# Kernel optimization log

Measured on AMD Instinct MI355X. Metric: run time of the kernel, lower is better.

## Reference

```python
import jax, jax.numpy as jnp
import numpy as np

B, C, H, W = 1, 256, 64, 64
K_DIM, V_DIM, HEADS = 64, 64, 8


def setup_inputs() -> dict:
    key = jax.random.key(0)
    ks = jax.random.split(key, 13)
    s = lambda i, shape: jax.random.normal(ks[i], shape, dtype=jnp.float32) * 0.05
    return {
        "x": s(0, (B, C, H, W)),
        # low-rank bottleneck projections (bias=False), torch Linear weight is [out,in]
        "wq1": s(1, (K_DIM // 2, C)),
        "wk1": s(2, (K_DIM // 2, C)),
        "wv1": s(3, (V_DIM // 2, C)),
        # expansion to per-head dims (bias=False)
        "wq2": s(4, (K_DIM * HEADS, K_DIM // 2)),
        "wk2": s(5, (K_DIM * HEADS, K_DIM // 2)),
        "wv2": s(6, (V_DIM * HEADS, V_DIM // 2)),
        # output projection (with bias)
        "wo": s(7, (C, V_DIM * HEADS)),
        "bo": s(8, (C,)),
        # depthwise 3x3 conv (groups=C): [C,1,3,3]
        "w_dw": s(9, (C, 1, 3, 3)),
        "b_dw": s(10, (C,)),
        # 1x1 gate conv
        "w_gate": s(11, (C, C, 1, 1)),
        "b_gate": s(12, (C,)),
    }


def reference(x, wq1, wk1, wv1, wq2, wk2, wv2, wo, bo, w_dw, b_dw, w_gate, b_gate):
    B_, C_, H_, W_ = x.shape
    N = H_ * W_
    t = x.transpose(0, 2, 3, 1).reshape(B_, N, C_)  # [B, N, C]
    # low-rank then expansion: Linear(x) = x @ W.T
    q = (t @ wq1.T) @ wq2.T  # [B, N, HEADS*K_DIM]
    k = (t @ wk1.T) @ wk2.T
    v = (t @ wv1.T) @ wv2.T
    q = q.reshape(B_, N, HEADS, K_DIM).transpose(0, 2, 1, 3)  # [B,h,N,dk]
    k = k.reshape(B_, N, HEADS, K_DIM).transpose(0, 2, 1, 3)
    v = v.reshape(B_, N, HEADS, V_DIM).transpose(0, 2, 1, 3)
    attn = jnp.einsum('bhnd,bhmd->bhnm', q, k) / jnp.sqrt(jnp.float32(K_DIM))
    attn = jax.nn.softmax(attn, axis=-1)
    out = jnp.einsum('bhnm,bhmd->bhnd', attn, v)  # [B,h,N,dv]
    out = out.transpose(0, 2, 1, 3).reshape(B_, N, HEADS * V_DIM)
    out = out @ wo.T + bo  # [B, N, C]
    out = out.reshape(B_, H_, W_, C_).transpose(0, 3, 1, 2)  # NCHW
    dn = ('NCHW', 'OIHW', 'NCHW')
    out = jax.lax.conv_general_dilated(out, w_dw, (1, 1), 'SAME', dimension_numbers=dn,
                                       feature_group_count=C_) + b_dw[None, :, None, None]
    gate = jax.nn.sigmoid(
        jax.lax.conv_general_dilated(out, w_gate, (1, 1), 'SAME', dimension_numbers=dn)
        + b_gate[None, :, None, None])
    return out * gate
```

## Files before the change

kernel.cpp:

```cpp
#include <hip/hip_runtime.h>

typedef __bf16 bf16;
typedef __bf16 bf16x4 __attribute__((ext_vector_type(4)));
typedef __bf16 bf16x8 __attribute__((ext_vector_type(8)));
typedef float f32x4 __attribute__((ext_vector_type(4)));

#define MFMA16(a, b, c) __builtin_amdgcn_mfma_f32_16x16x32_bf16((a), (b), (c), 0, 0, 0)

__device__ inline float fexp2(float x) {
    float r;
    asm("v_exp_f32 %0, %1" : "=v"(r) : "v"(x));
    return r;
}

__global__ void k_transpose_x(const float* __restrict__ x, bf16* __restrict__ xt) {
    __shared__ float tile[64][68];
    const int t = threadIdx.x;
    const int c0 = (blockIdx.x & 3) * 64;
    const int n0 = (blockIdx.x >> 2) * 64;
    {
        const int cr = t >> 4, nc = (t & 15) * 4;
#pragma unroll
        for (int i = 0; i < 4; ++i) {
            const float4 v = *(const float4*)(x + (size_t)(c0 + cr + i * 16) * 4096 + n0 + nc);
            tile[cr + i * 16][nc + 0] = v.x;
            tile[cr + i * 16][nc + 1] = v.y;
            tile[cr + i * 16][nc + 2] = v.z;
            tile[cr + i * 16][nc + 3] = v.w;
        }
    }
    __syncthreads();
    const int n = t >> 2, cc = (t & 3) * 16;
    bf16x8 o0, o1;
#pragma unroll
    for (int j = 0; j < 8; ++j) o0[j] = (bf16)tile[cc + j][n];
#pragma unroll
    for (int j = 0; j < 8; ++j) o1[j] = (bf16)tile[cc + 8 + j][n];
    bf16* dst = xt + (size_t)(n0 + n) * 256 + c0 + cc;
    *(bf16x8*)dst = o0;
    *(bf16x8*)(dst + 8) = o1;
}

__global__ void k_prep_w(const float* __restrict__ wq1, const float* __restrict__ wk1,
                         const float* __restrict__ wv1, const float* __restrict__ wq2,
                         const float* __restrict__ wk2, const float* __restrict__ wv2,
                         const float* __restrict__ wo, const float* __restrict__ wg,
                         bf16* __restrict__ Wq, bf16* __restrict__ Wk, bf16* __restrict__ Wv,
                         bf16* __restrict__ wo_bf, bf16* __restrict__ wg_bf) {
    int t = blockIdx.x * 256 + threadIdx.x;
    if (t < 393216) {
        int which = t >> 17;
        int rem = t & 131071;
        int o = rem >> 8, c = rem & 255;
        const float* w1 = which == 0 ? wq1 : which == 1 ? wk1 : wv1;
        const float* w2 = which == 0 ? wq2 : which == 1 ? wk2 : wv2;
        float acc = 0.f;
#pragma unroll
        for (int j = 0; j < 32; ++j) acc += w2[o * 32 + j] * w1[j * 256 + c];
        bf16* W = which == 0 ? Wq : which == 1 ? Wk : Wv;
        W[o * 256 + c] = (bf16)acc;
    } else if (t < 524288) {
        int idx = t - 393216;
        wo_bf[idx] = (bf16)wo[idx];
    } else if (t < 589824) {
        int idx = t - 524288;
        wg_bf[idx] = (bf16)wg[idx];
    }
}

template <int MODE>
__launch_bounds__(256)
__global__ void k_gemm_nt(const bf16* __restrict__ A, const bf16* __restrict__ B,
                          int K, float scale, void* __restrict__ outp,
                          const float* __restrict__ bias, const float* __restrict__ mul) {
    const int lane = threadIdx.x & 63;
    const int w = threadIdx.x >> 6;
    const int i0 = blockIdx.y * 128 + w * 32;
    const int j0 = blockIdx.x * 64;
    const int lrow = lane & 15;
    const int lk = (lane >> 4) * 8;

    f32x4 acc[2][4];
#pragma unroll
    for (int a = 0; a < 2; ++a)
#pragma unroll
        for (int b = 0; b < 4; ++b) acc[a][b] = (f32x4){0.f, 0.f, 0.f, 0.f};

    for (int k0 = 0; k0 < K; k0 += 32) {
        bf16x8 af[2], bfr[4];
#pragma unroll
        for (int qs = 0; qs < 2; ++qs)
            af[qs] = *(const bf16x8*)(A + (size_t)(i0 + qs * 16 + lrow) * K + k0 + lk);
#pragma unroll
        for (int js = 0; js < 4; ++js)
            bfr[js] = *(const bf16x8*)(B + (size_t)(j0 + js * 16 + lrow) * K + k0 + lk);
#pragma unroll
        for (int qs = 0; qs < 2; ++qs)
#pragma unroll
            for (int js = 0; js < 4; ++js)
                acc[qs][js] = MFMA16(af[qs], bfr[js], acc[qs][js]);
    }

    const int rbase = (lane >> 4) * 4;
#pragma unroll
    for (int qs = 0; qs < 2; ++qs)
#pragma unroll
        for (int js = 0; js < 4; ++js)
#pragma unroll
            for (int r = 0; r < 4; ++r) {
                int i = i0 + qs * 16 + rbase + r;
                int j = j0 + js * 16 + lrow;
                float v = acc[qs][js][r];
                if (MODE == 0) {
                    ((bf16*)outp)[(size_t)(j >> 6) * (4096 * 64) + (size_t)i * 64 + (j & 63)] =
                        (bf16)(v * scale);
                } else if (MODE == 1) {
                    ((bf16*)outp)[(size_t)i * 4096 + j] = (bf16)v;
                } else if (MODE == 2) {
                    ((float*)outp)[(size_t)i * 4096 + j] = v + bias[i];
                } else {
                    float g = v + bias[i];
                    float sg = 1.f / (1.f + __expf(-g));
                    ((float*)outp)[(size_t)i * 4096 + j] = mul[(size_t)i * 4096 + j] * sg;
                }
            }
}

__launch_bounds__(256)
__global__ void k_attn(const bf16* __restrict__ q, const bf16* __restrict__ k,
                       const bf16* __restrict__ vT, bf16* __restrict__ Opart,
                       float* __restrict__ lpart) {
    __shared__ char kvlds[16384];
    __shared__ char plds[4][4096];
    const int tid = threadIdx.x;
    const int lane = tid & 63;
    const int w = tid >> 6;
    const int split = blockIdx.x >> 8;
    const int h = (blockIdx.x >> 5) & 7;
    const int qt = blockIdx.x & 31;
    const int qbase = qt * 128 + w * 32;
    const int lrow = lane & 15;
    const int g = lane >> 4;
    const int swzr = (lrow & 7) << 4;

    const bf16* qh = q + (size_t)h * 4096 * 64;
    const bf16* kh = k + (size_t)h * 4096 * 64;
    const bf16* vh = vT + (size_t)h * 64 * 4096;
    char* myp = plds[w];
    const char* Kl = kvlds;
    const char* Vl = kvlds + 8192;

    const int isV = tid >> 7;
    const int srow = (tid & 127) >> 1;
    const int shalf = tid & 1;
    const int swzs = (srow & 7) << 4;
    char* ldst = kvlds + isV * 8192 + srow * 128;
    const bf16* sbase = isV ? (vh + (size_t)srow * 4096 + split * 1024 + shalf * 32)
                            : (kh + ((size_t)split * 1024 + srow) * 64 + shalf * 32);
    const size_t sstep = isV ? 64 : 64 * 64;

    bf16x8 bq[2][2];
#pragma unroll
    for (int qs = 0; qs < 2; ++qs)
#pragma unroll
        for (int ks = 0; ks < 2; ++ks)
            bq[qs][ks] = *(const bf16x8*)(qh + (size_t)(qbase + qs * 16 + lrow) * 64 +
                                          ks * 32 + g * 8);

    f32x4 accO[2][4];
    float lsum[2] = {0.f, 0.f};
#pragma unroll
    for (int qs = 0; qs < 2; ++qs)
#pragma unroll
        for (int ds = 0; ds < 4; ++ds) accO[qs][ds] = (f32x4){0.f, 0.f, 0.f, 0.f};

    uint4 r0, r1, r2, r3;
    {
        const bf16* p = sbase;
        r0 = *(const uint4*)(p);
        r1 = *(const uint4*)(p + 8);
        r2 = *(const uint4*)(p + 16);
        r3 = *(const uint4*)(p + 24);
    }

    for (int t = 0; t < 16; ++t) {
        *(uint4*)(ldst + ((shalf * 64 + 0) ^ swzs)) = r0;
        *(uint4*)(ldst + ((shalf * 64 + 16) ^ swzs)) = r1;
        *(uint4*)(ldst + ((shalf * 64 + 32) ^ swzs)) = r2;
        *(uint4*)(ldst + ((shalf * 64 + 48) ^ swzs)) = r3;
        if (t < 15) {
            const bf16* p = sbase + (size_t)(t + 1) * sstep;
            r0 = *(const uint4*)(p);
            r1 = *(const uint4*)(p + 8);
            r2 = *(const uint4*)(p + 16);
            r3 = *(const uint4*)(p + 24);
        }
        __syncthreads();

#pragma unroll
        for (int qs = 0; qs < 2; ++qs) {
            const int qrow = qs * 16 + lrow;
            f32x4 s[4];
#pragma unroll
            for (int js = 0; js < 4; ++js) s[js] = (f32x4){0.f, 0.f, 0.f, 0.f};
#pragma unroll
            for (int ks = 0; ks < 2; ++ks) {
                bf16x8 ak[4];
#pragma unroll
                for (int js = 0; js < 4; ++js)
                    ak[js] = *(const bf16x8*)(Kl + (js * 16 + lrow) * 128 +
                                              ((ks * 64 + g * 16) ^ swzr));
#pragma unroll
                for (int js = 0; js < 4; ++js)
                    s[js] = MFMA16(ak[js], bq[qs][ks], s[js]);
            }
#pragma unroll
            for (int js = 0; js < 4; ++js) {
                bf16x4 pk;
#pragma unroll
                for (int r = 0; r < 4; ++r) {
                    float e = fexp2(s[js][r]);
                    lsum[qs] += e;
                    pk[r] = (bf16)e;
                }
                *(bf16x4*)(myp + ((qrow * 128 + js * 32 + g * 8) ^ swzr)) = pk;
            }
#pragma unroll
            for (int ks2 = 0; ks2 < 2; ++ks2) {
                bf16x8 ap = *(const bf16x8*)(myp + ((qrow * 128 + ks2 * 64 + g * 16) ^ swzr));
                bf16x8 bv[4];
#pragma unroll
                for (int ds = 0; ds < 4; ++ds)
                    bv[ds] = *(const bf16x8*)(Vl + (ds * 16 + lrow) * 128 +
                                              ((ks2 * 64 + g * 16) ^ swzr));
#pragma unroll
                for (int ds = 0; ds < 4; ++ds)
                    accO[qs][ds] = MFMA16(ap, bv[ds], accO[qs][ds]);
            }
        }
        __syncthreads();
    }

#pragma unroll
    for (int qs = 0; qs < 2; ++qs)
#pragma unroll
        for (int ds = 0; ds < 4; ++ds)
#pragma unroll
            for (int r = 0; r < 4; ++r) {
                const int n = qbase + qs * 16 + 4 * g + r;
                Opart[((size_t)split * 4096 + n) * 512 + h * 64 + ds * 16 + lrow] =
                    (bf16)accO[qs][ds][r];
            }
#pragma unroll
    for (int qs = 0; qs < 2; ++qs) {
        float lv = lsum[qs];
        lv += __shfl_xor(lv, 16);
        lv += __shfl_xor(lv, 32);
        if (lane < 16)
            lpart[((size_t)split * 8 + h) * 4096 + qbase + qs * 16 + lane] = lv;
    }
}

__global__ void k_combine(const bf16* __restrict__ Opart, const float* __restrict__ lpart,
                          bf16* __restrict__ o) {
    const int tid = blockIdx.x * 256 + threadIdx.x;
    const int n = tid >> 6;
    const int c8 = (tid & 63) * 8;
    const int h = c8 >> 6;
    float acc[8] = {0, 0, 0, 0, 0, 0, 0, 0};
    float l = 0.f;
#pragma unroll
    for (int s = 0; s < 4; ++s) {
        const bf16x8 v = *(const bf16x8*)(Opart + ((size_t)s * 4096 + n) * 512 + c8);
#pragma unroll
        for (int j = 0; j < 8; ++j) acc[j] += (float)v[j];
        l += lpart[((size_t)s * 8 + h) * 4096 + n];
    }
    const float inv = 1.f / l;
    bf16x8 ov;
#pragma unroll
    for (int j = 0; j < 8; ++j) ov[j] = (bf16)(acc[j] * inv);
    *(bf16x8*)(o + (size_t)n * 512 + c8) = ov;
}

__global__ void k_dw(const float* __restrict__ y, const float* __restrict__ wdw,
                     const float* __restrict__ bdw, float* __restrict__ dwout,
                     bf16* __restrict__ dwt) {
    int t = blockIdx.x * 256 + threadIdx.x;
    int c = t >> 12, n = t & 4095, yy = n >> 6, xx = n & 63;
    float acc = bdw[c];
    const float* yc = y + (size_t)c * 4096;
#pragma unroll
    for (int ky = 0; ky < 3; ++ky) {
        int ry = yy + ky - 1;
        if ((unsigned)ry < 64u) {
#pragma unroll
            for (int kx = 0; kx < 3; ++kx) {
                int rx = xx + kx - 1;
                if ((unsigned)rx < 64u) acc += wdw[c * 9 + ky * 3 + kx] * yc[ry * 64 + rx];
            }
        }
    }
    dwout[t] = acc;
    dwt[n * 256 + c] = (bf16)acc;
}

extern "C" void kernel_launch(void* const* d_in, const int* in_sizes, int n_in,
                              void* d_out, int out_size, void* d_ws, size_t ws_size,
                              hipStream_t stream) {
    const float* x   = (const float*)d_in[0];
    const float* wq1 = (const float*)d_in[1];
    const float* wk1 = (const float*)d_in[2];
    const float* wv1 = (const float*)d_in[3];
    const float* wq2 = (const float*)d_in[4];
    const float* wk2 = (const float*)d_in[5];
    const float* wv2 = (const float*)d_in[6];
    const float* wo  = (const float*)d_in[7];
    const float* bo  = (const float*)d_in[8];
    const float* wdw = (const float*)d_in[9];
    const float* bdw = (const float*)d_in[10];
    const float* wg  = (const float*)d_in[11];
    const float* bg  = (const float*)d_in[12];

    char* ws = (char*)d_ws;
    size_t off = 0;
    auto alloc = [&](size_t bytes) {
        char* p = ws + off;
        off += (bytes + 255) & ~(size_t)255;
        return p;
    };
    bf16*  q_buf = (bf16*)alloc((size_t)8 * 4096 * 64 * 2);
    bf16*  k_buf = (bf16*)alloc((size_t)8 * 4096 * 64 * 2);
    bf16*  vT    = (bf16*)alloc((size_t)8 * 64 * 4096 * 2);
    bf16*  o_buf = (bf16*)alloc((size_t)4096 * 512 * 2);
    bf16*  wo_bf = (bf16*)alloc((size_t)256 * 512 * 2);
    bf16*  wg_bf = (bf16*)alloc((size_t)256 * 256 * 2);
    char* U = ws + off;
    bf16*  xbf = (bf16*)U;
    bf16*  Wq  = (bf16*)(U + (size_t)2 * 1024 * 1024);
    bf16*  Wk  = (bf16*)(U + (size_t)2 * 1024 * 1024 + 262144);
    bf16*  Wv  = (bf16*)(U + (size_t)2 * 1024 * 1024 + 524288);
    bf16*  Opart = (bf16*)U;
    float* lpart = (float*)(U + (size_t)16 * 1024 * 1024);
    float* ybuf  = (float*)U;
    float* dwout = (float*)(U + (size_t)4 * 1024 * 1024);
    bf16*  dwt   = (bf16*)(U + (size_t)8 * 1024 * 1024);
    (void)ws_size; (void)in_sizes; (void)n_in; (void)out_size;

    const float QSCALE = 0.125f * 1.4426950408889634f;

    k_transpose_x<<<256, 256, 0, stream>>>(x, xbf);
    k_prep_w<<<2304, 256, 0, stream>>>(wq1, wk1, wv1, wq2, wk2, wv2, wo, wg,
                                       Wq, Wk, Wv, wo_bf, wg_bf);
    k_gemm_nt<0><<<dim3(8, 32), 256, 0, stream>>>(xbf, Wq, 256, QSCALE, q_buf, nullptr, nullptr);
    k_gemm_nt<0><<<dim3(8, 32), 256, 0, stream>>>(xbf, Wk, 256, 1.0f, k_buf, nullptr, nullptr);
    k_gemm_nt<1><<<dim3(64, 4), 256, 0, stream>>>(Wv, xbf, 256, 1.0f, vT, nullptr, nullptr);
    k_attn<<<1024, 256, 0, stream>>>(q_buf, k_buf, vT, Opart, lpart);
    k_combine<<<1024, 256, 0, stream>>>(Opart, lpart, o_buf);
    k_gemm_nt<2><<<dim3(64, 2), 256, 0, stream>>>(wo_bf, o_buf, 512, 1.0f, ybuf, bo, nullptr);
    k_dw<<<4096, 256, 0, stream>>>(ybuf, wdw, bdw, dwout, dwt);
    k_gemm_nt<3><<<dim3(64, 2), 256, 0, stream>>>(wg_bf, dwt, 256, 1.0f, d_out, bg, dwout);
}
```

Baseline: 128.1 us.

## Double-buffer K/V tiles in attention, MFMA row sums, merge prep kernels

The attention kernel now double-buffers its K/V shared-memory tiles. The next tile is written into the alternate buffer while the current one is consumed, which removes one barrier per iteration. The per-row softmax denominator is now accumulated with an extra MFMA against a vector of ones instead of scalar adds in the exp loop. This takes VALU work off the loop but uses the bf16-rounded probabilities for the sum. The x-transpose and weight-prep kernels are merged into one launch to save a kernel launch. Shared memory grows by 16 KB per block, which may reduce occupancy.

Result: no change. 127.0 us (-0.9%).

```diff
diff --git a/kernel.cpp b/kernel.cpp
--- a/kernel.cpp
+++ b/kernel.cpp
@@ -13,58 +13,60 @@
     return r;
 }
 
-__global__ void k_transpose_x(const float* __restrict__ x, bf16* __restrict__ xt) {
+__global__ void k_pre(const float* __restrict__ x, bf16* __restrict__ xt,
+                      const float* __restrict__ wq1, const float* __restrict__ wk1,
+                      const float* __restrict__ wv1, const float* __restrict__ wq2,
+                      const float* __restrict__ wk2, const float* __restrict__ wv2,
+                      const float* __restrict__ wo, const float* __restrict__ wg,
+                      bf16* __restrict__ Wq, bf16* __restrict__ Wk, bf16* __restrict__ Wv,
+                      bf16* __restrict__ wo_bf, bf16* __restrict__ wg_bf) {
     __shared__ float tile[64][68];
-    const int t = threadIdx.x;
-    const int c0 = (blockIdx.x & 3) * 64;
-    const int n0 = (blockIdx.x >> 2) * 64;
-    {
-        const int cr = t >> 4, nc = (t & 15) * 4;
-#pragma unroll
-        for (int i = 0; i < 4; ++i) {
-            const float4 v = *(const float4*)(x + (size_t)(c0 + cr + i * 16) * 4096 + n0 + nc);
-            tile[cr + i * 16][nc + 0] = v.x;
-            tile[cr + i * 16][nc + 1] = v.y;
-            tile[cr + i * 16][nc + 2] = v.z;
-            tile[cr + i * 16][nc + 3] = v.w;
-        }
-    }
-    __syncthreads();
-    const int n = t >> 2, cc = (t & 3) * 16;
-    bf16x8 o0, o1;
-#pragma unroll
-    for (int j = 0; j < 8; ++j) o0[j] = (bf16)tile[cc + j][n];
-#pragma unroll
-    for (int j = 0; j < 8; ++j) o1[j] = (bf16)tile[cc + 8 + j][n];
-    bf16* dst = xt + (size_t)(n0 + n) * 256 + c0 + cc;
-    *(bf16x8*)dst = o0;
-    *(bf16x8*)(dst + 8) = o1;
-}
-
-__global__ void k_prep_w(const float* __restrict__ wq1, const float* __restrict__ wk1,
-                         const float* __restrict__ wv1, const float* __restrict__ wq2,
-                         const float* __restrict__ wk2, const float* __restrict__ wv2,
-                         const float* __restrict__ wo, const float* __restrict__ wg,
-                         bf16* __restrict__ Wq, bf16* __restrict__ Wk, bf16* __restrict__ Wv,
-                         bf16* __restrict__ wo_bf, bf16* __restrict__ wg_bf) {
-    int t = blockIdx.x * 256 + threadIdx.x;
-    if (t < 393216) {
-        int which = t >> 17;
-        int rem = t & 131071;
-        int o = rem >> 8, c = rem & 255;
-        const float* w1 = which == 0 ? wq1 : which == 1 ? wk1 : wv1;
-        const float* w2 = which == 0 ? wq2 : which == 1 ? wk2 : wv2;
-        float acc = 0.f;
-#pragma unroll
-        for (int j = 0; j < 32; ++j) acc += w2[o * 32 + j] * w1[j * 256 + c];
-        bf16* W = which == 0 ? Wq : which == 1 ? Wk : Wv;
-        W[o * 256 + c] = (bf16)acc;
-    } else if (t < 524288) {
-        int idx = t - 393216;
-        wo_bf[idx] = (bf16)wo[idx];
-    } else if (t < 589824) {
-        int idx = t - 524288;
-        wg_bf[idx] = (bf16)wg[idx];
+    const int bx = blockIdx.x;
+    if (bx < 256) {
+        const int t = threadIdx.x;
+        const int c0 = (bx & 3) * 64;
+        const int n0 = (bx >> 2) * 64;
+        {
+            const int cr = t >> 4, nc = (t & 15) * 4;
+#pragma unroll
+            for (int i = 0; i < 4; ++i) {
+                const float4 v = *(const float4*)(x + (size_t)(c0 + cr + i * 16) * 4096 + n0 + nc);
+                tile[cr + i * 16][nc + 0] = v.x;
+                tile[cr + i * 16][nc + 1] = v.y;
+                tile[cr + i * 16][nc + 2] = v.z;
+                tile[cr + i * 16][nc + 3] = v.w;
+            }
+        }
+        __syncthreads();
+        const int n = t >> 2, cc = (t & 3) * 16;
+        bf16x8 o0, o1;
+#pragma unroll
+        for (int j = 0; j < 8; ++j) o0[j] = (bf16)tile[cc + j][n];
+#pragma unroll
+        for (int j = 0; j < 8; ++j) o1[j] = (bf16)tile[cc + 8 + j][n];
+        bf16* dst = xt + (size_t)(n0 + n) * 256 + c0 + cc;
+        *(bf16x8*)dst = o0;
+        *(bf16x8*)(dst + 8) = o1;
+    } else {
+        int t = (bx - 256) * 256 + threadIdx.x;
+        if (t < 393216) {
+            int which = t >> 17;
+            int rem = t & 131071;
+            int o = rem >> 8, c = rem & 255;
+            const float* w1 = which == 0 ? wq1 : which == 1 ? wk1 : wv1;
+            const float* w2 = which == 0 ? wq2 : which == 1 ? wk2 : wv2;
+            float acc = 0.f;
+#pragma unroll
+            for (int j = 0; j < 32; ++j) acc += w2[o * 32 + j] * w1[j * 256 + c];
+            bf16* W = which == 0 ? Wq : which == 1 ? Wk : Wv;
+            W[o * 256 + c] = (bf16)acc;
+        } else if (t < 524288) {
+            int idx = t - 393216;
+            wo_bf[idx] = (bf16)wo[idx];
+        } else if (t < 589824) {
+            int idx = t - 524288;
+            wg_bf[idx] = (bf16)wg[idx];
+        }
     }
 }
 
@@ -130,7 +132,7 @@
 __global__ void k_attn(const bf16* __restrict__ q, const bf16* __restrict__ k,
                        const bf16* __restrict__ vT, bf16* __restrict__ Opart,
                        float* __restrict__ lpart) {
-    __shared__ char kvlds[16384];
+    __shared__ char kvlds[2][16384];
     __shared__ char plds[4][4096];
     const int tid = threadIdx.x;
     const int lane = tid & 63;
@@ -147,14 +149,12 @@
     const bf16* kh = k + (size_t)h * 4096 * 64;
     const bf16* vh = vT + (size_t)h * 64 * 4096;
     char* myp = plds[w];
-    const char* Kl = kvlds;
-    const char* Vl = kvlds + 8192;
 
     const int isV = tid >> 7;
     const int srow = (tid & 127) >> 1;
     const int shalf = tid & 1;
     const int swzs = (srow & 7) << 4;
-    char* ldst = kvlds + isV * 8192 + srow * 128;
+    const int ldoff = isV * 8192 + srow * 128;
     const bf16* sbase = isV ? (vh + (size_t)srow * 4096 + split * 1024 + shalf * 32)
                             : (kh + ((size_t)split * 1024 + srow) * 64 + shalf * 32);
     const size_t sstep = isV ? 64 : 64 * 64;
@@ -168,11 +168,16 @@
                                           ks * 32 + g * 8);
 
     f32x4 accO[2][4];
-    float lsum[2] = {0.f, 0.f};
-#pragma unroll
-    for (int qs = 0; qs < 2; ++qs)
+    f32x4 l_acc[2];
+#pragma unroll
+    for (int qs = 0; qs < 2; ++qs) {
 #pragma unroll
         for (int ds = 0; ds < 4; ++ds) accO[qs][ds] = (f32x4){0.f, 0.f, 0.f, 0.f};
+        l_acc[qs] = (f32x4){0.f, 0.f, 0.f, 0.f};
+    }
+    bf16x8 ones;
+#pragma unroll
+    for (int i = 0; i < 8; ++i) ones[i] = (bf16)1.0f;
 
     uint4 r0, r1, r2, r3;
     {
@@ -182,20 +187,40 @@
         r2 = *(const uint4*)(p + 16);
         r3 = *(const uint4*)(p + 24);
     }
+    {
+        char* d = kvlds[0] + ldoff;
+        *(uint4*)(d + ((shalf * 64 + 0) ^ swzs)) = r0;
+        *(uint4*)(d + ((shalf * 64 + 16) ^ swzs)) = r1;
+        *(uint4*)(d + ((shalf * 64 + 32) ^ swzs)) = r2;
+        *(uint4*)(d + ((shalf * 64 + 48) ^ swzs)) = r3;
+    }
+    {
+        const bf16* p = sbase + sstep;
+        r0 = *(const uint4*)(p);
+        r1 = *(const uint4*)(p + 8);
+        r2 = *(const uint4*)(p + 16);
+        r3 = *(const uint4*)(p + 24);
+    }
+    __syncthreads();
 
     for (int t = 0; t < 16; ++t) {
-        *(uint4*)(ldst + ((shalf * 64 + 0) ^ swzs)) = r0;
-        *(uint4*)(ldst + ((shalf * 64 + 16) ^ swzs)) = r1;
-        *(uint4*)(ldst + ((shalf * 64 + 32) ^ swzs)) = r2;
-        *(uint4*)(ldst + ((shalf * 64 + 48) ^ swzs)) = r3;
+        const int cur = t & 1;
         if (t < 15) {
-            const bf16* p = sbase + (size_t)(t + 1) * sstep;
+            char* d = kvlds[cur ^ 1] + ldoff;
+            *(uint4*)(d + ((shalf * 64 + 0) ^ swzs)) = r0;
+            *(uint4*)(d + ((shalf * 64 + 16) ^ swzs)) = r1;
+            *(uint4*)(d + ((shalf * 64 + 32) ^ swzs)) = r2;
+            *(uint4*)(d + ((shalf * 64 + 48) ^ swzs)) = r3;
+        }
+        if (t < 14) {
+            const bf16* p = sbase + (size_t)(t + 2) * sstep;
             r0 = *(const uint4*)(p);
             r1 = *(const uint4*)(p + 8);
             r2 = *(const uint4*)(p + 16);
             r3 = *(const uint4*)(p + 24);
         }
-        __syncthreads();
+        const char* Kl = kvlds[cur];
+        const char* Vl = kvlds[cur] + 8192;
 
 #pragma unroll
         for (int qs = 0; qs < 2; ++qs) {
@@ -218,11 +243,7 @@
             for (int js = 0; js < 4; ++js) {
                 bf16x4 pk;
 #pragma unroll
-                for (int r = 0; r < 4; ++r) {
-                    float e = fexp2(s[js][r]);
-                    lsum[qs] += e;
-                    pk[r] = (bf16)e;
-                }
+                for (int r = 0; r < 4; ++r) pk[r] = (bf16)fexp2(s[js][r]);
                 *(bf16x4*)(myp + ((qrow * 128 + js * 32 + g * 8) ^ swzr)) = pk;
             }
 #pragma unroll
@@ -236,6 +257,7 @@
 #pragma unroll
                 for (int ds = 0; ds < 4; ++ds)
                     accO[qs][ds] = MFMA16(ap, bv[ds], accO[qs][ds]);
+                l_acc[qs] = MFMA16(ap, ones, l_acc[qs]);
             }
         }
         __syncthreads();
@@ -251,13 +273,13 @@
                 Opart[((size_t)split * 4096 + n) * 512 + h * 64 + ds * 16 + lrow] =
                     (bf16)accO[qs][ds][r];
             }
-#pragma unroll
-    for (int qs = 0; qs < 2; ++qs) {
-        float lv = lsum[qs];
-        lv += __shfl_xor(lv, 16);
-        lv += __shfl_xor(lv, 32);
-        if (lane < 16)
-            lpart[((size_t)split * 8 + h) * 4096 + qbase + qs * 16 + lane] = lv;
+    if (lrow == 0) {
+#pragma unroll
+        for (int qs = 0; qs < 2; ++qs)
+#pragma unroll
+            for (int r = 0; r < 4; ++r)
+                lpart[((size_t)split * 8 + h) * 4096 + qbase + qs * 16 + 4 * g + r] =
+                    l_acc[qs][r];
     }
 }
 
@@ -349,9 +371,8 @@
 
     const float QSCALE = 0.125f * 1.4426950408889634f;
 
-    k_transpose_x<<<256, 256, 0, stream>>>(x, xbf);
-    k_prep_w<<<2304, 256, 0, stream>>>(wq1, wk1, wv1, wq2, wk2, wv2, wo, wg,
-                                       Wq, Wk, Wv, wo_bf, wg_bf);
+    k_pre<<<2560, 256, 0, stream>>>(x, xbf, wq1, wk1, wv1, wq2, wk2, wv2, wo, wg,
+                                    Wq, Wk, Wv, wo_bf, wg_bf);
     k_gemm_nt<0><<<dim3(8, 32), 256, 0, stream>>>(xbf, Wq, 256, QSCALE, q_buf, nullptr, nullptr);
     k_gemm_nt<0><<<dim3(8, 32), 256, 0, stream>>>(xbf, Wk, 256, 1.0f, k_buf, nullptr, nullptr);
     k_gemm_nt<1><<<dim3(64, 4), 256, 0, stream>>>(Wv, xbf, 256, 1.0f, vT, nullptr, nullptr);
```
